# Kernel optimization log

Hardware: AMD Instinct MI355X
Metric: run time of the kernel (lower is better)

## Reference

```python
import jax, jax.numpy as jnp
import numpy as np
from functools import partial

EMB = 768
ATTN = 768
HEADS = 12
N = 4096
K = 64
ALPHA = 0.5
TEMP = 0.5
THRESH = 1e-4
MAX_ITER = 100
DKM_EPS = 1e-6
LN_EPS = 1e-5


def setup_inputs() -> dict:
    key = jax.random.key(0)
    ks = jax.random.split(key, 12)
    s = 0.02
    return {
        "original_embeddings": jax.random.normal(ks[0], (N, EMB), jnp.float32),
        "fc1_w": jax.random.normal(ks[1], (ATTN, EMB), jnp.float32) * s,
        "fc1_b": jnp.zeros((ATTN,), jnp.float32),
        "fc2_w": jax.random.normal(ks[2], (EMB, ATTN), jnp.float32) * s,
        "fc2_b": jnp.zeros((EMB,), jnp.float32),
        "in_proj_w": jax.random.normal(ks[3], (3 * ATTN, ATTN), jnp.float32) * s,
        "in_proj_b": jnp.zeros((3 * ATTN,), jnp.float32),
        "out_w": jax.random.normal(ks[4], (ATTN, ATTN), jnp.float32) * s,
        "out_b": jnp.zeros((ATTN,), jnp.float32),
        "ln_g": jnp.ones((EMB,), jnp.float32),
        "ln_b": jnp.zeros((EMB,), jnp.float32),
        "init_idx": jax.random.randint(ks[5], (K,), 0, N, jnp.int64 if jax.config.jax_enable_x64 else jnp.int32),
        "k_cl": K,
    }


def _cdist(x, c):
    # squared euclidean via expansion, clipped for numerical safety
    sq = (jnp.sum(x * x, 1)[:, None] + jnp.sum(c * c, 1)[None, :]
          - 2.0 * (x @ c.T))
    return jnp.sqrt(jnp.maximum(sq, 0.0))


def _dkm_step(X, C):
    a = jax.nn.softmax(-_cdist(X, C) / TEMP, axis=1)   # [N, K]
    a_sum = jnp.sum(a, axis=0) + DKM_EPS               # [K]
    C_new = (a.T @ X) / a_sum[:, None]                 # [K, D]
    return a, C_new


def _transform(x, fc1_w, fc1_b, fc2_w, fc2_b, in_proj_w, in_proj_b, out_w, out_b, ln_g, ln_b):
    h = jax.nn.relu(x @ fc1_w.T + fc1_b)               # [N, A]
    qkv = h @ in_proj_w.T + in_proj_b                  # [N, 3A]
    q, k, v = jnp.split(qkv, 3, axis=1)
    hd = ATTN // HEADS
    q = q.reshape(N, HEADS, hd).transpose(1, 0, 2)     # [H, N, hd]
    k = k.reshape(N, HEADS, hd).transpose(1, 0, 2)
    v = v.reshape(N, HEADS, hd).transpose(1, 0, 2)
    scores = jnp.einsum('hnd,hmd->hnm', q, k) / np.sqrt(hd).astype(np.float32)
    attn = jax.nn.softmax(scores, axis=-1)             # [H, N, N]
    o = jnp.einsum('hnm,hmd->hnd', attn, v)            # [H, N, hd]
    o = o.transpose(1, 0, 2).reshape(N, ATTN)
    o = o @ out_w.T + out_b
    y = jax.nn.relu(o @ fc2_w.T + fc2_b)               # [N, E]
    z = (1.0 - ALPHA) * x + ALPHA * y
    mu = jnp.mean(z, axis=-1, keepdims=True)
    var = jnp.mean((z - mu) ** 2, axis=-1, keepdims=True)
    return (z - mu) / jnp.sqrt(var + LN_EPS) * ln_g + ln_b


def reference(original_embeddings, fc1_w, fc1_b, fc2_w, fc2_b,
              in_proj_w, in_proj_b, out_w, out_b, ln_g, ln_b,
              init_idx, k_cl):
    X = _transform(original_embeddings, fc1_w, fc1_b, fc2_w, fc2_b,
                   in_proj_w, in_proj_b, out_w, out_b, ln_g, ln_b)
    C0 = X[init_idx]                                   # [K, E]
    a0, C1 = _dkm_step(X, C0)
    diff0 = jnp.sum(jnp.abs(C1 - C0))

    def cond(st):
        _, _, _, diff, i = st
        return (diff > THRESH) & (i < MAX_ITER)

    def body(st):
        _, _, C_new, _, i = st
        C = C_new
        a, C_new2 = _dkm_step(X, C)
        diff = jnp.sum(jnp.abs(C_new2 - C))
        return (C, a, C_new2, diff, i + 1)

    C, a, _, _, _ = jax.lax.while_loop(cond, body, (C0, a0, C1, diff0, jnp.int32(0)))
    return C, a
```

## Files before the change

### kernel.cpp

```cpp
#include <hip/hip_runtime.h>
#include <cstdint>

typedef __bf16 bf16;
typedef __bf16 bf16x4 __attribute__((ext_vector_type(4)));
typedef __bf16 bf16x8 __attribute__((ext_vector_type(8)));
typedef float  f32x4  __attribute__((ext_vector_type(4)));

#define LOG2E 1.44269504088896340736f

__device__ __forceinline__ f32x4 mfma16(bf16x8 a, bf16x8 b, f32x4 c) {
  return __builtin_amdgcn_mfma_f32_16x16x32_bf16(a, b, c, 0, 0, 0);
}

__device__ __forceinline__ void gl2lds16(const bf16* g, bf16* l) {
  __builtin_amdgcn_global_load_lds(
      (const __attribute__((address_space(1))) unsigned int*)g,
      (__attribute__((address_space(3))) unsigned int*)l, 16, 0, 0);
}

__global__ __launch_bounds__(256) void cvt_all(
    const float* __restrict__ x0, const float* __restrict__ w1,
    const float* __restrict__ w2, const float* __restrict__ wip,
    const float* __restrict__ wo,
    bf16* __restrict__ dx0, bf16* __restrict__ dw1, bf16* __restrict__ dw2,
    bf16* __restrict__ dwip, bf16* __restrict__ dwo, float* __restrict__ ctrl)
{
  int i = blockIdx.x * 256 + threadIdx.x;
  if (blockIdx.x == 0) {
    for (int u = threadIdx.x; u < 8192; u += 256) ctrl[u] = 0.f;
  }
  const float* s; bf16* d; int base;
  if      (i <  786432) { s = x0;  d = dx0;  base = 0; }
  else if (i <  933888) { s = w1;  d = dw1;  base = 786432; }
  else if (i < 1081344) { s = w2;  d = dw2;  base = 933888; }
  else if (i < 1523712) { s = wip; d = dwip; base = 1081344; }
  else                  { s = wo;  d = dwo;  base = 1523712; }
  int j = i - base;
  f32x4 v = ((const f32x4*)s)[j];
  bf16x4 r;
  r[0] = (bf16)v[0]; r[1] = (bf16)v[1]; r[2] = (bf16)v[2]; r[3] = (bf16)v[3];
  ((bf16x4*)d)[j] = r;
}

template<int RELU, int OUTF32>
__global__ __launch_bounds__(256) void gemm128(
    const bf16* __restrict__ A, const bf16* __restrict__ W,
    const float* __restrict__ bias, bf16* __restrict__ outb,
    float* __restrict__ outf, int N)
{
  __shared__ bf16 Ab[2][8192];
  __shared__ bf16 Bb[2][8192];
  const int tid = threadIdx.x;
  const int w = tid >> 6, lane = tid & 63;
  const int q2 = lane >> 4, c = lane & 15;
  const int wrow = (w >> 1) * 64, wcol = (w & 1) * 64;
  const int mb = blockIdx.x * 128, nb = blockIdx.y * 128;
  const int srow = tid >> 3, sgrp = tid & 7;

  auto stage = [&](const bf16* __restrict__ src, int rowbase, int kb, bf16* dst) {
#pragma unroll
    for (int i = 0; i < 4; ++i) {
      int row = i * 32 + srow;
      int gs = (sgrp ^ (row & 7)) * 8;
      gl2lds16(src + (size_t)(rowbase + row) * 768 + kb + gs,
               dst + i * 2048 + tid * 8);
    }
  };

  f32x4 acc[4][4] = {};
  stage(A, mb, 0, Ab[0]);
  stage(W, nb, 0, Bb[0]);
  for (int kb = 0; kb < 12; ++kb) {
    const int buf = kb & 1;
    __syncthreads();
    if (kb < 11) {
      stage(A, mb, (kb + 1) * 64, Ab[buf ^ 1]);
      stage(W, nb, (kb + 1) * 64, Bb[buf ^ 1]);
    }
#pragma unroll
    for (int kc = 0; kc < 2; ++kc) {
      bf16x8 af[4], bfr[4];
#pragma unroll
      for (int rt = 0; rt < 4; ++rt) {
        int r = wrow + rt * 16 + c;
        af[rt] = *(const bf16x8*)&Ab[buf][r * 64 + (((kc * 4 + q2) ^ (r & 7)) * 8)];
      }
#pragma unroll
      for (int ct = 0; ct < 4; ++ct) {
        int r = wcol + ct * 16 + c;
        bfr[ct] = *(const bf16x8*)&Bb[buf][r * 64 + (((kc * 4 + q2) ^ (r & 7)) * 8)];
      }
#pragma unroll
      for (int rt = 0; rt < 4; ++rt)
#pragma unroll
        for (int ct = 0; ct < 4; ++ct)
          acc[rt][ct] = mfma16(af[rt], bfr[ct], acc[rt][ct]);
    }
  }
#pragma unroll
  for (int rt = 0; rt < 4; ++rt) {
#pragma unroll
    for (int ct = 0; ct < 4; ++ct) {
      int col = nb + wcol + ct * 16 + c;
      float bv = bias[col];
#pragma unroll
      for (int j = 0; j < 4; ++j) {
        int row = mb + wrow + rt * 16 + q2 * 4 + j;
        float v = acc[rt][ct][j] + bv;
        if (RELU) v = fmaxf(v, 0.f);
        if (OUTF32) outf[(size_t)row * N + col] = v;
        else        outb[(size_t)row * N + col] = (bf16)v;
      }
    }
  }
}

__global__ __launch_bounds__(256) void transpose_bf16(
    const bf16* __restrict__ src, bf16* __restrict__ dst,
    int stride, int colOff, int dstride)
{
  __shared__ bf16 t[64][72];
  const int br = blockIdx.x, bc = blockIdx.y;
  {
    int ir = threadIdx.x >> 2, icb = (threadIdx.x & 3) * 16;
    const bf16* srow = src + (size_t)(br * 64 + ir) * stride + colOff + bc * 64 + icb;
    *(bf16x8*)&t[ir][icb] = *(const bf16x8*)srow;
    *(bf16x8*)&t[ir][icb + 8] = *(const bf16x8*)(srow + 8);
  }
  __syncthreads();
  {
    int oc = threadIdx.x >> 2, orb = (threadIdx.x & 3) * 16;
    bf16x8 v0, v1;
#pragma unroll
    for (int j = 0; j < 8; ++j) { v0[j] = t[orb + j][oc]; v1[j] = t[orb + 8 + j][oc]; }
    bf16* drow = dst + (size_t)(bc * 64 + oc) * dstride + br * 64 + orb;
    *(bf16x8*)drow = v0;
    *(bf16x8*)(drow + 8) = v1;
  }
}

__global__ __launch_bounds__(256) void attn_kernel(
    const bf16* __restrict__ qkv, const bf16* __restrict__ vt, bf16* __restrict__ o)
{
  const int h = blockIdx.x >> 6;
  const int qt = blockIdx.x & 63;
  const int w = threadIdx.x >> 6, lane = threadIdx.x & 63;
  const int q2 = lane >> 4, c = lane & 15;
  const int qbase = qt * 64 + w * 16;
  __shared__ bf16 Ks[2][64][64];
  __shared__ bf16 Vs[2][64][64];
  __shared__ bf16 Pl[4][16][72];

  const bf16* Qr = qkv + (size_t)(qbase + c) * 2304 + h * 64 + q2 * 8;
  bf16x8 a0 = *(const bf16x8*)(Qr);
  bf16x8 a1 = *(const bf16x8*)(Qr + 32);

  const int srow = lane >> 3;
  const int sg = ((lane & 7) ^ srow) * 8;
  const bf16* kg = qkv + (size_t)(w * 16 + srow) * 2304 + 768 + h * 64 + sg;
  const bf16* vg = vt + (size_t)(h * 64 + w * 16 + srow) * 4096 + sg;

  auto stage = [&](int jt, int buf) {
    const int kvb = jt * 64;
    gl2lds16(kg + (size_t)kvb * 2304,       &Ks[buf][w * 16][0]);
    gl2lds16(kg + (size_t)(kvb + 8) * 2304, &Ks[buf][w * 16 + 8][0]);
    gl2lds16(vg + kvb,                      &Vs[buf][w * 16][0]);
    gl2lds16(vg + kvb + 8 * 4096,           &Vs[buf][w * 16 + 8][0]);
  };

  bf16x8 ones;
#pragma unroll
  for (int i = 0; i < 8; ++i) ones[i] = (bf16)1.0f;

  f32x4 oa[4] = {};
  f32x4 accl = {};
  const int gsw = (q2 ^ (c & 7)) * 8;
  const float SC = 0.125f * LOG2E;

  stage(0, 0);
  for (int jt = 0; jt < 64; ++jt) {
    const int buf = jt & 1;
    __syncthreads();
    if (jt < 63) stage(jt + 1, buf ^ 1);
    f32x4 s[4];
#pragma unroll
    for (int nt = 0; nt < 4; ++nt) {
      const int row = nt * 16 + c;
      bf16x8 b0 = *(const bf16x8*)&Ks[buf][row][gsw];
      bf16x8 b1 = *(const bf16x8*)&Ks[buf][row][gsw ^ 32];
      f32x4 t = {};
      t = mfma16(a0, b0, t);
      t = mfma16(a1, b1, t);
      s[nt] = t;
    }
#pragma unroll
    for (int nt = 0; nt < 4; ++nt)
#pragma unroll
      for (int j = 0; j < 4; ++j)
        Pl[w][q2 * 4 + j][nt * 16 + c] = (bf16)exp2f(s[nt][j] * SC);
    bf16x8 p0 = *(const bf16x8*)(&Pl[w][c][q2 * 8]);
    bf16x8 p1 = *(const bf16x8*)(&Pl[w][c][32 + q2 * 8]);
    accl = mfma16(p0, ones, accl);
    accl = mfma16(p1, ones, accl);
#pragma unroll
    for (int dt = 0; dt < 4; ++dt) {
      const int row = dt * 16 + c;
      bf16x8 v0 = *(const bf16x8*)&Vs[buf][row][gsw];
      bf16x8 v1 = *(const bf16x8*)&Vs[buf][row][gsw ^ 32];
      oa[dt] = mfma16(p0, v0, oa[dt]);
      oa[dt] = mfma16(p1, v1, oa[dt]);
    }
  }
#pragma unroll
  for (int dt = 0; dt < 4; ++dt)
#pragma unroll
    for (int j = 0; j < 4; ++j) {
      int row = qbase + q2 * 4 + j;
      int col = h * 64 + dt * 16 + c;
      o[(size_t)row * 768 + col] = (bf16)(oa[dt][j] / accl[j]);
    }
}

__global__ __launch_bounds__(256) void ln_kernel(
    const float* __restrict__ x0, const float* __restrict__ y,
    const float* __restrict__ g, const float* __restrict__ b,
    float* __restrict__ X, bf16* __restrict__ Xb, float* __restrict__ xn2)
{
  const int w = threadIdx.x >> 6, lane = threadIdx.x & 63;
  const int row = blockIdx.x * 4 + w;
  const float* xr = x0 + (size_t)row * 768;
  const float* yr = y + (size_t)row * 768;
  float z[12]; float s = 0.f;
#pragma unroll
  for (int i = 0; i < 12; ++i) {
    int col = lane + i * 64;
    float zz = 0.5f * xr[col] + 0.5f * yr[col];
    z[i] = zz; s += zz;
  }
#pragma unroll
  for (int off = 32; off; off >>= 1) s += __shfl_xor(s, off, 64);
  float mu = s * (1.f / 768.f);
  float v = 0.f;
#pragma unroll
  for (int i = 0; i < 12; ++i) { float d = z[i] - mu; v += d * d; }
#pragma unroll
  for (int off = 32; off; off >>= 1) v += __shfl_xor(v, off, 64);
  float rstd = rsqrtf(v * (1.f / 768.f) + 1e-5f);
  float sn = 0.f;
#pragma unroll
  for (int i = 0; i < 12; ++i) {
    int col = lane + i * 64;
    float xv = (z[i] - mu) * rstd * g[col] + b[col];
    X[(size_t)row * 768 + col] = xv;
    Xb[(size_t)row * 768 + col] = (bf16)xv;
    sn += xv * xv;
  }
#pragma unroll
  for (int off = 32; off; off >>= 1) sn += __shfl_xor(sn, off, 64);
  if (lane == 0) xn2[row] = sn;
}

__device__ __forceinline__ void gridbar(int* bar, int& ep, int g) {
  __syncthreads();
  if (threadIdx.x == 0) {
    ep++;
    __builtin_amdgcn_fence(__ATOMIC_RELEASE, "agent");
    int v = __hip_atomic_fetch_add(bar + g * 64, 1, __ATOMIC_RELAXED,
                                   __HIP_MEMORY_SCOPE_AGENT) + 1;
    if (v == 32 * ep) {
      int tv = __hip_atomic_fetch_add(bar + 512, 1, __ATOMIC_RELAXED,
                                      __HIP_MEMORY_SCOPE_AGENT) + 1;
      if (tv == 8 * ep) {
#pragma unroll
        for (int i = 0; i < 8; ++i)
          __hip_atomic_store(bar + 1024 + i * 64, ep, __ATOMIC_RELAXED,
                             __HIP_MEMORY_SCOPE_AGENT);
      }
    }
    long guard = 0;
    while (__hip_atomic_load(bar + 1024 + g * 64, __ATOMIC_RELAXED,
                             __HIP_MEMORY_SCOPE_AGENT) < ep) {
      __builtin_amdgcn_s_sleep(2);
      if (++guard > (1L << 28)) break;
    }
    __builtin_amdgcn_fence(__ATOMIC_ACQUIRE, "agent");
  }
  __syncthreads();
}

__global__ __launch_bounds__(256) void dkm_fused(
    const float* __restrict__ XF, const int* __restrict__ idx,
    const bf16* __restrict__ Xb, const bf16* __restrict__ Xt,
    const float* __restrict__ xn2,
    float* __restrict__ CB, bf16* __restrict__ CBH,
    bf16* __restrict__ aT, float* __restrict__ a_out, float* __restrict__ outC,
    float* __restrict__ asumall, float* __restrict__ cnall,
    float* __restrict__ diffall, int* __restrict__ bar)
{
  extern __shared__ char dynsmem[];
  bf16* XtL = (bf16*)dynsmem;
  __shared__ bf16 XL[16][776];
  __shared__ float GsRed[1024];
  __shared__ float asl[64];
  __shared__ float cnl[16];
  __shared__ float dred[4];
  __shared__ float sdiff;
  float (*Gs)[64] = (float(*)[64])GsRed;
  float (*red)[16][16] = (float(*)[16][16])GsRed;
  const int tid = threadIdx.x;
  const int w = tid >> 6, lane = tid & 63;
  const int q2 = lane >> 4, c = lane & 15;
  const int b = blockIdx.x;
  const int g = b & 7;
  const int rbase = b * 16;
  const int tr = b / 48, tc = b % 48;
  int ep = 0;

  {
    int row = tid >> 4, seg = (tid & 15) * 48;
    const bf16* src = Xb + (size_t)(rbase + row) * 768 + seg;
#pragma unroll
    for (int i = 0; i < 6; ++i)
      *(bf16x8*)&XL[row][seg + i * 8] = *(const bf16x8*)(src + i * 8);
  }
  if (b < 192) {
    const int row = tid >> 4, cc = tid & 15;
    const bf16* XtS = Xt + (size_t)(tc * 16 + row) * 4096;
#pragma unroll
    for (int i = 0; i < 32; ++i) {
      int gg = i * 16 + cc;
      bf16x8 vv = *(const bf16x8*)(XtS + gg * 8);
      *(bf16x8*)&XtL[(size_t)row * 4096 + ((gg ^ (row & 7)) * 8)] = vv;
    }
  }
  if (b < 64) {
    const int src = idx[b];
    float s = 0.f;
#pragma unroll
    for (int u = 0; u < 3; ++u) {
      int d = u * 256 + tid;
      float v = XF[(size_t)src * 768 + d];
      CB[(size_t)b * 768 + d] = v;
      CBH[(size_t)b * 768 + d] = (bf16)v;
      s += v * v;
    }
#pragma unroll
    for (int off = 32; off; off >>= 1) s += __shfl_xor(s, off, 64);
    if (lane == 0) dred[w] = s;
    __syncthreads();
    if (tid == 0) cnall[b] = dred[0] + dred[1] + dred[2] + dred[3];
  }
  const int arow = tid >> 4, aci = tid & 15;
  const float xn = xn2[rbase + arow];
  gridbar(bar, ep, g);

  int p = 0;
  for (int t = 0; t < 100; ++t) {
    const int par = t & 1;
    {
      if (b == 0) {
        if (tid >= 128 && tid < 192) asumall[(par ^ 1) * 64 + tid - 128] = 0.f;
        else if (tid >= 192)         cnall[(par ^ 1) * 64 + tid - 192] = 0.f;
      }
      const bf16* C = CBH + (size_t)par * 49152;
      const float* cnp = cnall + par * 64;
      const bf16* Cr = C + (size_t)(w * 16 + c) * 768 + q2 * 8;
      f32x4 a0 = {}, a1 = {}, a2 = {}, a3 = {};
#pragma unroll
      for (int ks = 0; ks < 24; ks += 4) {
        a0 = mfma16(*(const bf16x8*)&XL[c][q2 * 8 + ks * 32],
                    *(const bf16x8*)(Cr + ks * 32), a0);
        a1 = mfma16(*(const bf16x8*)&XL[c][q2 * 8 + (ks + 1) * 32],
                    *(const bf16x8*)(Cr + (ks + 1) * 32), a1);
        a2 = mfma16(*(const bf16x8*)&XL[c][q2 * 8 + (ks + 2) * 32],
                    *(const bf16x8*)(Cr + (ks + 2) * 32), a2);
        a3 = mfma16(*(const bf16x8*)&XL[c][q2 * 8 + (ks + 3) * 32],
                    *(const bf16x8*)(Cr + (ks + 3) * 32), a3);
      }
      f32x4 acc = (a0 + a1) + (a2 + a3);
      if (tid < 64) asl[tid] = 0.f;
#pragma unroll
      for (int j = 0; j < 4; ++j) Gs[q2 * 4 + j][w * 16 + c] = acc[j];
      __syncthreads();
      float lg[4];
#pragma unroll
      for (int u = 0; u < 4; ++u) {
        int col = aci + u * 16;
        float d2 = xn + cnp[col] - 2.f * Gs[arow][col];
        lg[u] = -2.f * sqrtf(fmaxf(d2, 0.f));
      }
      float mx = fmaxf(fmaxf(lg[0], lg[1]), fmaxf(lg[2], lg[3]));
#pragma unroll
      for (int off = 8; off; off >>= 1) mx = fmaxf(mx, __shfl_xor(mx, off, 16));
      float sum = 0.f;
#pragma unroll
      for (int u = 0; u < 4; ++u) { float e = exp2f((lg[u] - mx) * LOG2E); lg[u] = e; sum += e; }
#pragma unroll
      for (int off = 8; off; off >>= 1) sum += __shfl_xor(sum, off, 16);
      float rs = 1.f / sum;
#pragma unroll
      for (int u = 0; u < 4; ++u) {
        int col = aci + u * 16;
        float av = lg[u] * rs;
        aT[(size_t)col * 4096 + rbase + arow] = (bf16)av;
        atomicAdd(&asl[col], av);
      }
      __syncthreads();
      if (tid < 64) atomicAdd(&asumall[par * 64 + tid], asl[tid]);
    }
    gridbar(bar, ep, g);
    if (b < 192) {
      const bf16* Ar = aT + (size_t)(tr * 16 + c) * 4096 + q2 * 8;
      f32x4 b0 = {}, b1 = {}, b2 = {}, b3 = {};
#pragma unroll
      for (int i = 0; i < 32; i += 4) {
#pragma unroll
        for (int u = 0; u < 4; ++u) {
          int ii = i + u;
          int kb = (w + ii * 4) * 32;
          int gb = (w + ii * 4) * 4 + q2;
          bf16x8 bv = *(const bf16x8*)&XtL[(size_t)c * 4096 + ((gb ^ (c & 7)) * 8)];
          bf16x8 av = *(const bf16x8*)(Ar + kb);
          if (u == 0) b0 = mfma16(av, bv, b0);
          else if (u == 1) b1 = mfma16(av, bv, b1);
          else if (u == 2) b2 = mfma16(av, bv, b2);
          else b3 = mfma16(av, bv, b3);
        }
      }
      f32x4 acc = (b0 + b1) + (b2 + b3);
#pragma unroll
      for (int j = 0; j < 4; ++j) red[w][q2 * 4 + j][c] = acc[j];
      if (tid < 16) cnl[tid] = 0.f;
      __syncthreads();
      const int r = tid >> 4, cl = tid & 15;
      float s = red[0][r][cl] + red[1][r][cl] + red[2][r][cl] + red[3][r][cl];
      const int cluster = tr * 16 + r, dcol = tc * 16 + cl;
      float denom = asumall[par * 64 + cluster] + 1e-6f;
      float cnew = s / denom;
      size_t cidx = (size_t)cluster * 768 + dcol;
      float cold = CB[(size_t)par * 49152 + cidx];
      CB[(size_t)(par ^ 1) * 49152 + cidx] = cnew;
      CBH[(size_t)(par ^ 1) * 49152 + cidx] = (bf16)cnew;
      atomicAdd(&cnl[r], cnew * cnew);
      float dv = fabsf(cnew - cold);
#pragma unroll
      for (int off = 32; off; off >>= 1) dv += __shfl_xor(dv, off, 64);
      if (lane == 0) dred[w] = dv;
      __syncthreads();
      if (tid < 16)
        atomicAdd(&cnall[(par ^ 1) * 64 + tr * 16 + tid], cnl[tid]);
      if (tid == 0)
        atomicAdd(&diffall[par], dred[0] + dred[1] + dred[2] + dred[3]);
    } else if (b == 255 && tid == 0) {
      diffall[par ^ 1] = 0.f;
    }
    gridbar(bar, ep, g);
    if (tid == 0)
      sdiff = *(volatile const float*)&diffall[par];
    __syncthreads();
    if (sdiff <= 1e-4f) { p = par; break; }
    p = (t + 1) & 1;
  }
  {
    const bf16* C = CBH + (size_t)p * 49152;
    const float* cnp = cnall + p * 64;
    f32x4 acc = {};
    const bf16* Cr = C + (size_t)(w * 16 + c) * 768 + q2 * 8;
#pragma unroll
    for (int ks = 0; ks < 24; ++ks) {
      bf16x8 a = *(const bf16x8*)&XL[c][q2 * 8 + ks * 32];
      bf16x8 bb = *(const bf16x8*)(Cr + ks * 32);
      acc = mfma16(a, bb, acc);
    }
    __syncthreads();
#pragma unroll
    for (int j = 0; j < 4; ++j) Gs[q2 * 4 + j][w * 16 + c] = acc[j];
    __syncthreads();
    float lg[4];
#pragma unroll
    for (int u = 0; u < 4; ++u) {
      int col = aci + u * 16;
      float d2 = xn + cnp[col] - 2.f * Gs[arow][col];
      lg[u] = -2.f * sqrtf(fmaxf(d2, 0.f));
    }
    float mx = fmaxf(fmaxf(lg[0], lg[1]), fmaxf(lg[2], lg[3]));
#pragma unroll
    for (int off = 8; off; off >>= 1) mx = fmaxf(mx, __shfl_xor(mx, off, 16));
    float sum = 0.f;
#pragma unroll
    for (int u = 0; u < 4; ++u) { float e = exp2f((lg[u] - mx) * LOG2E); lg[u] = e; sum += e; }
#pragma unroll
    for (int off = 8; off; off >>= 1) sum += __shfl_xor(sum, off, 16);
    float rs = 1.f / sum;
#pragma unroll
    for (int u = 0; u < 4; ++u)
      a_out[(size_t)(rbase + arow) * 64 + aci + u * 16] = lg[u] * rs;
  }
  if (tid < 192) outC[b * 192 + tid] = CB[(size_t)p * 49152 + b * 192 + tid];
}

extern "C" void kernel_launch(void* const* d_in, const int* in_sizes, int n_in,
                              void* d_out, int out_size, void* d_ws, size_t ws_size,
                              hipStream_t stream) {
  const float* x0   = (const float*)d_in[0];
  const float* fc1w = (const float*)d_in[1];
  const float* fc1b = (const float*)d_in[2];
  const float* fc2w = (const float*)d_in[3];
  const float* fc2b = (const float*)d_in[4];
  const float* ipw  = (const float*)d_in[5];
  const float* ipb  = (const float*)d_in[6];
  const float* outw = (const float*)d_in[7];
  const float* outbias = (const float*)d_in[8];
  const float* lng  = (const float*)d_in[9];
  const float* lnb  = (const float*)d_in[10];
  const int*   idx  = (const int*)d_in[11];

  char* p = (char*)d_ws;
  auto take = [&](size_t n) { char* r = p; p += (n + 255) & ~(size_t)255; return r; };
  bf16* X0B   = (bf16*)take((size_t)4096 * 768 * 2);
  bf16* W1B   = (bf16*)take((size_t)768 * 768 * 2);
  bf16* FC2WB = (bf16*)take((size_t)768 * 768 * 2);
  bf16* IPWB  = (bf16*)take((size_t)2304 * 768 * 2);
  bf16* OUTWB = (bf16*)take((size_t)768 * 768 * 2);
  bf16* HB    = (bf16*)take((size_t)4096 * 768 * 2);
  bf16* QKVB  = (bf16*)take((size_t)4096 * 2304 * 2);
  bf16* VT    = (bf16*)take((size_t)768 * 4096 * 2);
  bf16* OB    = (bf16*)take((size_t)4096 * 768 * 2);
  bf16* O2B   = (bf16*)take((size_t)4096 * 768 * 2);
  float* YF   = (float*)take((size_t)4096 * 768 * 4);
  float* XF   = (float*)take((size_t)4096 * 768 * 4);
  bf16* XBB   = (bf16*)take((size_t)4096 * 768 * 2);
  bf16* XTB   = (bf16*)take((size_t)768 * 4096 * 2);
  float* XN2  = (float*)take((size_t)4096 * 4);
  float* CB   = (float*)take((size_t)2 * 49152 * 4);
  bf16* CBH   = (bf16*)take((size_t)2 * 49152 * 2);
  bf16* ATB   = (bf16*)take((size_t)64 * 4096 * 2);
  float* CTRLF = (float*)take(8192 * 4);
  float* ASUM = CTRLF;
  float* CN   = CTRLF + 128;
  float* DIFF = CTRLF + 256;
  int* BAR    = (int*)(CTRLF + 512);

  float* aout = (float*)d_out + 49152;

  cvt_all<<<6528, 256, 0, stream>>>(x0, fc1w, fc2w, ipw, outw,
                                    X0B, W1B, FC2WB, IPWB, OUTWB, CTRLF);
  gemm128<1, 0><<<dim3(32, 6), 256, 0, stream>>>(X0B, W1B, fc1b, HB, nullptr, 768);
  gemm128<0, 0><<<dim3(32, 18), 256, 0, stream>>>(HB, IPWB, ipb, QKVB, nullptr, 2304);
  transpose_bf16<<<dim3(64, 12), 256, 0, stream>>>(QKVB, VT, 2304, 1536, 4096);
  attn_kernel<<<768, 256, 0, stream>>>(QKVB, VT, OB);
  gemm128<0, 0><<<dim3(32, 6), 256, 0, stream>>>(OB, OUTWB, outbias, O2B, nullptr, 768);
  gemm128<1, 1><<<dim3(32, 6), 256, 0, stream>>>(O2B, FC2WB, fc2b, nullptr, YF, 768);
  ln_kernel<<<1024, 256, 0, stream>>>(x0, YF, lng, lnb, XF, XBB, XN2);
  transpose_bf16<<<dim3(64, 12), 256, 0, stream>>>(XBB, XTB, 768, 0, 4096);
  dkm_fused<<<256, 256, 131072, stream>>>(XF, idx, XBB, XTB, XN2, CB, CBH, ATB, aout,
                                          (float*)d_out, ASUM, CN, DIFF, BAR);
}
```

Baseline: 541.4 us.

## Fuse V transpose into QKV GEMM, register-shuffle P in attention, drop fp32 X

The QKV GEMM epilogue now also writes the transposed V slice directly, which removes one transpose kernel launch and its memory traffic. The attention kernel swaps MFMA operand order so the score tile comes out transposed, and it moves P between lanes with ds_bpermute instead of a round trip through shared memory. The LayerNorm no longer writes an fp32 copy of X, and the DKM initial centroids are read from the bf16 X instead. In exchange, the initial centroids are now rounded to bf16, which could change the clustering trajectory slightly, and the VT stores from the GEMM epilogue are small 8-byte scattered writes.

```diff
diff --git a/kernel.cpp b/kernel.cpp
--- a/kernel.cpp
+++ b/kernel.cpp
@@ -16,6 +16,12 @@
   __builtin_amdgcn_global_load_lds(
       (const __attribute__((address_space(1))) unsigned int*)g,
       (__attribute__((address_space(3))) unsigned int*)l, 16, 0, 0);
+}
+
+__device__ __forceinline__ int pack_bf16x2(float lo, float hi) {
+  union { bf16 h[2]; int i; } u;
+  u.h[0] = (bf16)lo; u.h[1] = (bf16)hi;
+  return u.i;
 }
 
 __global__ __launch_bounds__(256) void cvt_all(
@@ -42,11 +48,11 @@
   ((bf16x4*)d)[j] = r;
 }
 
-template<int RELU, int OUTF32>
+template<int RELU, int OUTF32, int WRITEVT>
 __global__ __launch_bounds__(256) void gemm128(
     const bf16* __restrict__ A, const bf16* __restrict__ W,
     const float* __restrict__ bias, bf16* __restrict__ outb,
-    float* __restrict__ outf, int N)
+    float* __restrict__ outf, int N, bf16* __restrict__ vtout)
 {
   __shared__ bf16 Ab[2][8192];
   __shared__ bf16 Bb[2][8192];
@@ -103,13 +109,18 @@
     for (int ct = 0; ct < 4; ++ct) {
       int col = nb + wcol + ct * 16 + c;
       float bv = bias[col];
+      bf16x4 vv;
 #pragma unroll
       for (int j = 0; j < 4; ++j) {
         int row = mb + wrow + rt * 16 + q2 * 4 + j;
         float v = acc[rt][ct][j] + bv;
         if (RELU) v = fmaxf(v, 0.f);
         if (OUTF32) outf[(size_t)row * N + col] = v;
-        else        outb[(size_t)row * N + col] = (bf16)v;
+        else { outb[(size_t)row * N + col] = (bf16)v; vv[j] = (bf16)v; }
+      }
+      if (WRITEVT && col >= 1536) {
+        int row0 = mb + wrow + rt * 16 + q2 * 4;
+        *(bf16x4*)&vtout[(size_t)(col - 1536) * 4096 + row0] = vv;
       }
     }
   }
@@ -149,7 +160,6 @@
   const int qbase = qt * 64 + w * 16;
   __shared__ bf16 Ks[2][64][64];
   __shared__ bf16 Vs[2][64][64];
-  __shared__ bf16 Pl[4][16][72];
 
   const bf16* Qr = qkv + (size_t)(qbase + c) * 2304 + h * 64 + q2 * 8;
   bf16x8 a0 = *(const bf16x8*)(Qr);
@@ -176,55 +186,79 @@
   f32x4 accl = {};
   const int gsw = (q2 ^ (c & 7)) * 8;
   const float SC = 0.125f * LOG2E;
+  const int L0 = ((q2 & 1) * 2 * 16 + c) * 4;
+  const int L1 = (((q2 & 1) * 2 + 1) * 16 + c) * 4;
+  const bool hi = (q2 & 2) != 0;
 
   stage(0, 0);
   for (int jt = 0; jt < 64; ++jt) {
     const int buf = jt & 1;
     __syncthreads();
     if (jt < 63) stage(jt + 1, buf ^ 1);
-    f32x4 s[4];
+    f32x4 st[4];
 #pragma unroll
     for (int nt = 0; nt < 4; ++nt) {
       const int row = nt * 16 + c;
-      bf16x8 b0 = *(const bf16x8*)&Ks[buf][row][gsw];
-      bf16x8 b1 = *(const bf16x8*)&Ks[buf][row][gsw ^ 32];
+      bf16x8 k0 = *(const bf16x8*)&Ks[buf][row][gsw];
+      bf16x8 k1 = *(const bf16x8*)&Ks[buf][row][gsw ^ 32];
       f32x4 t = {};
-      t = mfma16(a0, b0, t);
-      t = mfma16(a1, b1, t);
-      s[nt] = t;
-    }
-#pragma unroll
-    for (int nt = 0; nt < 4; ++nt)
-#pragma unroll
-      for (int j = 0; j < 4; ++j)
-        Pl[w][q2 * 4 + j][nt * 16 + c] = (bf16)exp2f(s[nt][j] * SC);
-    bf16x8 p0 = *(const bf16x8*)(&Pl[w][c][q2 * 8]);
-    bf16x8 p1 = *(const bf16x8*)(&Pl[w][c][32 + q2 * 8]);
-    accl = mfma16(p0, ones, accl);
-    accl = mfma16(p1, ones, accl);
+      t = mfma16(k0, a0, t);
+      t = mfma16(k1, a1, t);
+      st[nt] = t;
+    }
+    int pk[4][2];
+#pragma unroll
+    for (int nt = 0; nt < 4; ++nt) {
+      pk[nt][0] = pack_bf16x2(exp2f(st[nt][0] * SC), exp2f(st[nt][1] * SC));
+      pk[nt][1] = pack_bf16x2(exp2f(st[nt][2] * SC), exp2f(st[nt][3] * SC));
+    }
+    int r_lo[2][4], r_hi[2][4];
+#pragma unroll
+    for (int hh = 0; hh < 2; ++hh) {
+      r_lo[0][hh]     = __builtin_amdgcn_ds_bpermute(L0, pk[0][hh]);
+      r_hi[0][hh]     = __builtin_amdgcn_ds_bpermute(L0, pk[1][hh]);
+      r_lo[1][hh]     = __builtin_amdgcn_ds_bpermute(L1, pk[0][hh]);
+      r_hi[1][hh]     = __builtin_amdgcn_ds_bpermute(L1, pk[1][hh]);
+      r_lo[0][2 + hh] = __builtin_amdgcn_ds_bpermute(L0, pk[2][hh]);
+      r_hi[0][2 + hh] = __builtin_amdgcn_ds_bpermute(L0, pk[3][hh]);
+      r_lo[1][2 + hh] = __builtin_amdgcn_ds_bpermute(L1, pk[2][hh]);
+      r_hi[1][2 + hh] = __builtin_amdgcn_ds_bpermute(L1, pk[3][hh]);
+    }
+    union { int i[4]; bf16x8 v; } u0, u1;
+    u0.i[0] = hi ? r_hi[0][0] : r_lo[0][0];
+    u0.i[1] = hi ? r_hi[0][1] : r_lo[0][1];
+    u0.i[2] = hi ? r_hi[1][0] : r_lo[1][0];
+    u0.i[3] = hi ? r_hi[1][1] : r_lo[1][1];
+    u1.i[0] = hi ? r_hi[0][2] : r_lo[0][2];
+    u1.i[1] = hi ? r_hi[0][3] : r_lo[0][3];
+    u1.i[2] = hi ? r_hi[1][2] : r_lo[1][2];
+    u1.i[3] = hi ? r_hi[1][3] : r_lo[1][3];
+    bf16x8 p0 = u0.v, p1 = u1.v;
+    accl = mfma16(ones, p0, accl);
+    accl = mfma16(ones, p1, accl);
 #pragma unroll
     for (int dt = 0; dt < 4; ++dt) {
       const int row = dt * 16 + c;
       bf16x8 v0 = *(const bf16x8*)&Vs[buf][row][gsw];
       bf16x8 v1 = *(const bf16x8*)&Vs[buf][row][gsw ^ 32];
-      oa[dt] = mfma16(p0, v0, oa[dt]);
-      oa[dt] = mfma16(p1, v1, oa[dt]);
-    }
-  }
-#pragma unroll
-  for (int dt = 0; dt < 4; ++dt)
-#pragma unroll
-    for (int j = 0; j < 4; ++j) {
-      int row = qbase + q2 * 4 + j;
-      int col = h * 64 + dt * 16 + c;
-      o[(size_t)row * 768 + col] = (bf16)(oa[dt][j] / accl[j]);
-    }
+      oa[dt] = mfma16(v0, p0, oa[dt]);
+      oa[dt] = mfma16(v1, p1, oa[dt]);
+    }
+  }
+  const float inv = 1.f / accl[0];
+#pragma unroll
+  for (int dt = 0; dt < 4; ++dt) {
+    bf16x4 ov;
+#pragma unroll
+    for (int j = 0; j < 4; ++j) ov[j] = (bf16)(oa[dt][j] * inv);
+    *(bf16x4*)&o[(size_t)(qbase + c) * 768 + h * 64 + dt * 16 + q2 * 4] = ov;
+  }
 }
 
 __global__ __launch_bounds__(256) void ln_kernel(
     const float* __restrict__ x0, const float* __restrict__ y,
     const float* __restrict__ g, const float* __restrict__ b,
-    float* __restrict__ X, bf16* __restrict__ Xb, float* __restrict__ xn2)
+    bf16* __restrict__ Xb, float* __restrict__ xn2)
 {
   const int w = threadIdx.x >> 6, lane = threadIdx.x & 63;
   const int row = blockIdx.x * 4 + w;
@@ -251,7 +285,6 @@
   for (int i = 0; i < 12; ++i) {
     int col = lane + i * 64;
     float xv = (z[i] - mu) * rstd * g[col] + b[col];
-    X[(size_t)row * 768 + col] = xv;
     Xb[(size_t)row * 768 + col] = (bf16)xv;
     sn += xv * xv;
   }
@@ -289,7 +322,7 @@
 }
 
 __global__ __launch_bounds__(256) void dkm_fused(
-    const float* __restrict__ XF, const int* __restrict__ idx,
+    const int* __restrict__ idx,
     const bf16* __restrict__ Xb, const bf16* __restrict__ Xt,
     const float* __restrict__ xn2,
     float* __restrict__ CB, bf16* __restrict__ CBH,
@@ -339,9 +372,10 @@
 #pragma unroll
     for (int u = 0; u < 3; ++u) {
       int d = u * 256 + tid;
-      float v = XF[(size_t)src * 768 + d];
+      bf16 xv = Xb[(size_t)src * 768 + d];
+      float v = (float)xv;
       CB[(size_t)b * 768 + d] = v;
-      CBH[(size_t)b * 768 + d] = (bf16)v;
+      CBH[(size_t)b * 768 + d] = xv;
       s += v * v;
     }
 #pragma unroll
@@ -528,7 +562,6 @@
   bf16* OB    = (bf16*)take((size_t)4096 * 768 * 2);
   bf16* O2B   = (bf16*)take((size_t)4096 * 768 * 2);
   float* YF   = (float*)take((size_t)4096 * 768 * 4);
-  float* XF   = (float*)take((size_t)4096 * 768 * 4);
   bf16* XBB   = (bf16*)take((size_t)4096 * 768 * 2);
   bf16* XTB   = (bf16*)take((size_t)768 * 4096 * 2);
   float* XN2  = (float*)take((size_t)4096 * 4);
@@ -545,14 +578,13 @@
 
   cvt_all<<<6528, 256, 0, stream>>>(x0, fc1w, fc2w, ipw, outw,
                                     X0B, W1B, FC2WB, IPWB, OUTWB, CTRLF);
-  gemm128<1, 0><<<dim3(32, 6), 256, 0, stream>>>(X0B, W1B, fc1b, HB, nullptr, 768);
-  gemm128<0, 0><<<dim3(32, 18), 256, 0, stream>>>(HB, IPWB, ipb, QKVB, nullptr, 2304);
-  transpose_bf16<<<dim3(64, 12), 256, 0, stream>>>(QKVB, VT, 2304, 1536, 4096);
+  gemm128<1, 0, 0><<<dim3(32, 6), 256, 0, stream>>>(X0B, W1B, fc1b, HB, nullptr, 768, nullptr);
+  gemm128<0, 0, 1><<<dim3(32, 18), 256, 0, stream>>>(HB, IPWB, ipb, QKVB, nullptr, 2304, VT);
   attn_kernel<<<768, 256, 0, stream>>>(QKVB, VT, OB);
-  gemm128<0, 0><<<dim3(32, 6), 256, 0, stream>>>(OB, OUTWB, outbias, O2B, nullptr, 768);
-  gemm128<1, 1><<<dim3(32, 6), 256, 0, stream>>>(O2B, FC2WB, fc2b, nullptr, YF, 768);
-  ln_kernel<<<1024, 256, 0, stream>>>(x0, YF, lng, lnb, XF, XBB, XN2);
+  gemm128<0, 0, 0><<<dim3(32, 6), 256, 0, stream>>>(OB, OUTWB, outbias, O2B, nullptr, 768, nullptr);
+  gemm128<1, 1, 0><<<dim3(32, 6), 256, 0, stream>>>(O2B, FC2WB, fc2b, nullptr, YF, 768, nullptr);
+  ln_kernel<<<1024, 256, 0, stream>>>(x0, YF, lng, lnb, XBB, XN2);
   transpose_bf16<<<dim3(64, 12), 256, 0, stream>>>(XBB, XTB, 768, 0, 4096);
-  dkm_fused<<<256, 256, 131072, stream>>>(XF, idx, XBB, XTB, XN2, CB, CBH, ATB, aout,
+  dkm_fused<<<256, 256, 131072, stream>>>(idx, XBB, XTB, XN2, CB, CBH, ATB, aout,
                                           (float*)d_out, ASUM, CN, DIFF, BAR);
 }
```

After: 539.6 us (median of 2 runs). Within noise of the previous version (-0.3%).

## Fuse V transpose into QKV GEMM, double attention rows per block, drop fp32 X

Applied to the files above, without the earlier changes.

The QKV GEMM epilogue now also writes V transposed, so the separate transpose kernel goes away. The attention kernel processes 32 query rows per wave (128 per block), which halves the number of K/V tile loads, and launches 384 blocks instead of 768. The fp32 LayerNorm output buffer is removed and the initial centroids are gathered from the bf16 copy. This lowers kernel launches and memory traffic, but centroid initialisation loses precision, and the strided 4-element VT stores are uncoalesced.

```diff
diff --git a/kernel.cpp b/kernel.cpp
--- a/kernel.cpp
+++ b/kernel.cpp
@@ -42,11 +42,11 @@
   ((bf16x4*)d)[j] = r;
 }
 
-template<int RELU, int OUTF32>
+template<int RELU, int OUTF32, int WRITEVT>
 __global__ __launch_bounds__(256) void gemm128(
     const bf16* __restrict__ A, const bf16* __restrict__ W,
     const float* __restrict__ bias, bf16* __restrict__ outb,
-    float* __restrict__ outf, int N)
+    float* __restrict__ outf, int N, bf16* __restrict__ vtout)
 {
   __shared__ bf16 Ab[2][8192];
   __shared__ bf16 Bb[2][8192];
@@ -103,13 +103,18 @@
     for (int ct = 0; ct < 4; ++ct) {
       int col = nb + wcol + ct * 16 + c;
       float bv = bias[col];
+      bf16x4 vv;
 #pragma unroll
       for (int j = 0; j < 4; ++j) {
         int row = mb + wrow + rt * 16 + q2 * 4 + j;
         float v = acc[rt][ct][j] + bv;
         if (RELU) v = fmaxf(v, 0.f);
         if (OUTF32) outf[(size_t)row * N + col] = v;
-        else        outb[(size_t)row * N + col] = (bf16)v;
+        else { outb[(size_t)row * N + col] = (bf16)v; vv[j] = (bf16)v; }
+      }
+      if (WRITEVT && col >= 1536) {
+        int row0 = mb + wrow + rt * 16 + q2 * 4;
+        *(bf16x4*)&vtout[(size_t)(col - 1536) * 4096 + row0] = vv;
       }
     }
   }
@@ -142,18 +147,22 @@
 __global__ __launch_bounds__(256) void attn_kernel(
     const bf16* __restrict__ qkv, const bf16* __restrict__ vt, bf16* __restrict__ o)
 {
-  const int h = blockIdx.x >> 6;
-  const int qt = blockIdx.x & 63;
+  const int h = blockIdx.x >> 5;
+  const int qt = blockIdx.x & 31;
   const int w = threadIdx.x >> 6, lane = threadIdx.x & 63;
   const int q2 = lane >> 4, c = lane & 15;
-  const int qbase = qt * 64 + w * 16;
+  const int qbase = qt * 128 + w * 32;
   __shared__ bf16 Ks[2][64][64];
   __shared__ bf16 Vs[2][64][64];
-  __shared__ bf16 Pl[4][16][72];
-
-  const bf16* Qr = qkv + (size_t)(qbase + c) * 2304 + h * 64 + q2 * 8;
-  bf16x8 a0 = *(const bf16x8*)(Qr);
-  bf16x8 a1 = *(const bf16x8*)(Qr + 32);
+  __shared__ bf16 Pl[4][32][72];
+
+  bf16x8 a0[2], a1[2];
+#pragma unroll
+  for (int rg = 0; rg < 2; ++rg) {
+    const bf16* Qr = qkv + (size_t)(qbase + rg * 16 + c) * 2304 + h * 64 + q2 * 8;
+    a0[rg] = *(const bf16x8*)(Qr);
+    a1[rg] = *(const bf16x8*)(Qr + 32);
+  }
 
   const int srow = lane >> 3;
   const int sg = ((lane & 7) ^ srow) * 8;
@@ -172,8 +181,8 @@
 #pragma unroll
   for (int i = 0; i < 8; ++i) ones[i] = (bf16)1.0f;
 
-  f32x4 oa[4] = {};
-  f32x4 accl = {};
+  f32x4 oa[2][4] = {};
+  f32x4 accl[2] = {};
   const int gsw = (q2 ^ (c & 7)) * 8;
   const float SC = 0.125f * LOG2E;
 
@@ -182,49 +191,54 @@
     const int buf = jt & 1;
     __syncthreads();
     if (jt < 63) stage(jt + 1, buf ^ 1);
-    f32x4 s[4];
-#pragma unroll
-    for (int nt = 0; nt < 4; ++nt) {
-      const int row = nt * 16 + c;
-      bf16x8 b0 = *(const bf16x8*)&Ks[buf][row][gsw];
-      bf16x8 b1 = *(const bf16x8*)&Ks[buf][row][gsw ^ 32];
-      f32x4 t = {};
-      t = mfma16(a0, b0, t);
-      t = mfma16(a1, b1, t);
-      s[nt] = t;
-    }
-#pragma unroll
-    for (int nt = 0; nt < 4; ++nt)
-#pragma unroll
-      for (int j = 0; j < 4; ++j)
-        Pl[w][q2 * 4 + j][nt * 16 + c] = (bf16)exp2f(s[nt][j] * SC);
-    bf16x8 p0 = *(const bf16x8*)(&Pl[w][c][q2 * 8]);
-    bf16x8 p1 = *(const bf16x8*)(&Pl[w][c][32 + q2 * 8]);
-    accl = mfma16(p0, ones, accl);
-    accl = mfma16(p1, ones, accl);
-#pragma unroll
-    for (int dt = 0; dt < 4; ++dt) {
-      const int row = dt * 16 + c;
-      bf16x8 v0 = *(const bf16x8*)&Vs[buf][row][gsw];
-      bf16x8 v1 = *(const bf16x8*)&Vs[buf][row][gsw ^ 32];
-      oa[dt] = mfma16(p0, v0, oa[dt]);
-      oa[dt] = mfma16(p1, v1, oa[dt]);
-    }
-  }
-#pragma unroll
-  for (int dt = 0; dt < 4; ++dt)
-#pragma unroll
-    for (int j = 0; j < 4; ++j) {
-      int row = qbase + q2 * 4 + j;
-      int col = h * 64 + dt * 16 + c;
-      o[(size_t)row * 768 + col] = (bf16)(oa[dt][j] / accl[j]);
-    }
+#pragma unroll
+    for (int rg = 0; rg < 2; ++rg) {
+      f32x4 s[4];
+#pragma unroll
+      for (int nt = 0; nt < 4; ++nt) {
+        const int row = nt * 16 + c;
+        bf16x8 b0 = *(const bf16x8*)&Ks[buf][row][gsw];
+        bf16x8 b1 = *(const bf16x8*)&Ks[buf][row][gsw ^ 32];
+        f32x4 t = {};
+        t = mfma16(a0[rg], b0, t);
+        t = mfma16(a1[rg], b1, t);
+        s[nt] = t;
+      }
+#pragma unroll
+      for (int nt = 0; nt < 4; ++nt)
+#pragma unroll
+        for (int j = 0; j < 4; ++j)
+          Pl[w][rg * 16 + q2 * 4 + j][nt * 16 + c] = (bf16)exp2f(s[nt][j] * SC);
+      bf16x8 p0 = *(const bf16x8*)(&Pl[w][rg * 16 + c][q2 * 8]);
+      bf16x8 p1 = *(const bf16x8*)(&Pl[w][rg * 16 + c][32 + q2 * 8]);
+      accl[rg] = mfma16(p0, ones, accl[rg]);
+      accl[rg] = mfma16(p1, ones, accl[rg]);
+#pragma unroll
+      for (int dt = 0; dt < 4; ++dt) {
+        const int row = dt * 16 + c;
+        bf16x8 v0 = *(const bf16x8*)&Vs[buf][row][gsw];
+        bf16x8 v1 = *(const bf16x8*)&Vs[buf][row][gsw ^ 32];
+        oa[rg][dt] = mfma16(p0, v0, oa[rg][dt]);
+        oa[rg][dt] = mfma16(p1, v1, oa[rg][dt]);
+      }
+    }
+  }
+#pragma unroll
+  for (int rg = 0; rg < 2; ++rg)
+#pragma unroll
+    for (int dt = 0; dt < 4; ++dt)
+#pragma unroll
+      for (int j = 0; j < 4; ++j) {
+        int row = qbase + rg * 16 + q2 * 4 + j;
+        int col = h * 64 + dt * 16 + c;
+        o[(size_t)row * 768 + col] = (bf16)(oa[rg][dt][j] / accl[rg][j]);
+      }
 }
 
 __global__ __launch_bounds__(256) void ln_kernel(
     const float* __restrict__ x0, const float* __restrict__ y,
     const float* __restrict__ g, const float* __restrict__ b,
-    float* __restrict__ X, bf16* __restrict__ Xb, float* __restrict__ xn2)
+    bf16* __restrict__ Xb, float* __restrict__ xn2)
 {
   const int w = threadIdx.x >> 6, lane = threadIdx.x & 63;
   const int row = blockIdx.x * 4 + w;
@@ -251,7 +265,6 @@
   for (int i = 0; i < 12; ++i) {
     int col = lane + i * 64;
     float xv = (z[i] - mu) * rstd * g[col] + b[col];
-    X[(size_t)row * 768 + col] = xv;
     Xb[(size_t)row * 768 + col] = (bf16)xv;
     sn += xv * xv;
   }
@@ -289,7 +302,7 @@
 }
 
 __global__ __launch_bounds__(256) void dkm_fused(
-    const float* __restrict__ XF, const int* __restrict__ idx,
+    const int* __restrict__ idx,
     const bf16* __restrict__ Xb, const bf16* __restrict__ Xt,
     const float* __restrict__ xn2,
     float* __restrict__ CB, bf16* __restrict__ CBH,
@@ -339,9 +352,10 @@
 #pragma unroll
     for (int u = 0; u < 3; ++u) {
       int d = u * 256 + tid;
-      float v = XF[(size_t)src * 768 + d];
+      bf16 xv = Xb[(size_t)src * 768 + d];
+      float v = (float)xv;
       CB[(size_t)b * 768 + d] = v;
-      CBH[(size_t)b * 768 + d] = (bf16)v;
+      CBH[(size_t)b * 768 + d] = xv;
       s += v * v;
     }
 #pragma unroll
@@ -528,7 +542,6 @@
   bf16* OB    = (bf16*)take((size_t)4096 * 768 * 2);
   bf16* O2B   = (bf16*)take((size_t)4096 * 768 * 2);
   float* YF   = (float*)take((size_t)4096 * 768 * 4);
-  float* XF   = (float*)take((size_t)4096 * 768 * 4);
   bf16* XBB   = (bf16*)take((size_t)4096 * 768 * 2);
   bf16* XTB   = (bf16*)take((size_t)768 * 4096 * 2);
   float* XN2  = (float*)take((size_t)4096 * 4);
@@ -545,14 +558,13 @@
 
   cvt_all<<<6528, 256, 0, stream>>>(x0, fc1w, fc2w, ipw, outw,
                                     X0B, W1B, FC2WB, IPWB, OUTWB, CTRLF);
-  gemm128<1, 0><<<dim3(32, 6), 256, 0, stream>>>(X0B, W1B, fc1b, HB, nullptr, 768);
-  gemm128<0, 0><<<dim3(32, 18), 256, 0, stream>>>(HB, IPWB, ipb, QKVB, nullptr, 2304);
-  transpose_bf16<<<dim3(64, 12), 256, 0, stream>>>(QKVB, VT, 2304, 1536, 4096);
-  attn_kernel<<<768, 256, 0, stream>>>(QKVB, VT, OB);
-  gemm128<0, 0><<<dim3(32, 6), 256, 0, stream>>>(OB, OUTWB, outbias, O2B, nullptr, 768);
-  gemm128<1, 1><<<dim3(32, 6), 256, 0, stream>>>(O2B, FC2WB, fc2b, nullptr, YF, 768);
-  ln_kernel<<<1024, 256, 0, stream>>>(x0, YF, lng, lnb, XF, XBB, XN2);
+  gemm128<1, 0, 0><<<dim3(32, 6), 256, 0, stream>>>(X0B, W1B, fc1b, HB, nullptr, 768, nullptr);
+  gemm128<0, 0, 1><<<dim3(32, 18), 256, 0, stream>>>(HB, IPWB, ipb, QKVB, nullptr, 2304, VT);
+  attn_kernel<<<384, 256, 0, stream>>>(QKVB, VT, OB);
+  gemm128<0, 0, 0><<<dim3(32, 6), 256, 0, stream>>>(OB, OUTWB, outbias, O2B, nullptr, 768, nullptr);
+  gemm128<1, 1, 0><<<dim3(32, 6), 256, 0, stream>>>(O2B, FC2WB, fc2b, nullptr, YF, 768, nullptr);
+  ln_kernel<<<1024, 256, 0, stream>>>(x0, YF, lng, lnb, XBB, XN2);
   transpose_bf16<<<dim3(64, 12), 256, 0, stream>>>(XBB, XTB, 768, 0, 4096);
-  dkm_fused<<<256, 256, 131072, stream>>>(XF, idx, XBB, XTB, XN2, CB, CBH, ATB, aout,
+  dkm_fused<<<256, 256, 131072, stream>>>(idx, XBB, XTB, XN2, CB, CBH, ATB, aout,
                                           (float*)d_out, ASUM, CN, DIFF, BAR);
 }
```

After: 563.4 us. 4.1% more time.
